# Performance work log

Hardware: AMD Instinct MI355X
Metric: run time of the kernel (lower is better)

The kernel has to match this reference:

```python
import jax, jax.numpy as jnp
import numpy as np
import math

B, C, BINS, W = 2, 8, 1024, 512
HEADS = 16
HD = BINS // HEADS          # 64 head dim
ROT = BINS // HEADS // 2    # 32 rotated dims
EXP = 4
EPS = 1e-5
MAX_FREQ = 10.0


def setup_inputs() -> dict:
    key = jax.random.key(0)
    ks = jax.random.split(key, 8)
    def u(k, shape, fan_in):
        lim = 1.0 / math.sqrt(fan_in)
        return jax.random.uniform(k, shape, jnp.float32, -lim, lim)
    return {
        "x": jax.random.normal(ks[0], (B, C, BINS, W), jnp.float32),
        "norm1_w": jnp.ones((BINS,), jnp.float32),
        "norm1_b": jnp.zeros((BINS,), jnp.float32),
        # 'pixel' rotary init: linspace(1, max_freq/2, dim//2) * pi (learned)
        "rot_freqs": jnp.linspace(1.0, MAX_FREQ / 2, ROT // 2, dtype=jnp.float32) * math.pi,
        "q_w": u(ks[1], (C, BINS, BINS), BINS),
        "out_w": u(ks[2], (C, BINS, BINS), BINS),
        "norm2_w": jnp.ones((BINS,), jnp.float32),
        "norm2_b": jnp.zeros((BINS,), jnp.float32),
        "lin1_w": u(ks[3], (C, BINS * EXP, BINS), BINS),
        "lin2_w": u(ks[4], (C, BINS, BINS * EXP), BINS * EXP),
    }


def _mlin(x, w):
    # x: [b,c,f_in,w]; w: [c,f_out,f_in] -> [b,c,f_out,w]
    return jnp.einsum('bcfw,cgf->bcgw', x, w)


def _frame_norm(x, w, b):
    # LayerNorm over the bins axis (axis=2) of [b,c,bins,w]
    m = jnp.mean(x, axis=2, keepdims=True)
    v = jnp.var(x, axis=2, keepdims=True)
    xn = (x - m) * jax.lax.rsqrt(v + EPS)
    return xn * w[:, None] + b[:, None]


def _rotate(q, cos, sin):
    # q: [b,c,h,w,d]; rotate first ROT dims with interleaved-pair rotate_half
    q1, q2 = q[..., :ROT], q[..., ROT:]
    qp = q1.reshape(*q1.shape[:-1], ROT // 2, 2)
    rh = jnp.stack([-qp[..., 1], qp[..., 0]], axis=-1).reshape(q1.shape)
    return jnp.concatenate([q1 * cos + rh * sin, q2], axis=-1)


def _attention(x, rot_freqs, q_w, out_w):
    b, c, bins, w = x.shape
    # faithful to source: q, k, v ALL use q_proj
    y = _mlin(x, q_w)  # [b,c,bins,w]
    # -> [b,c,h,w,d]
    y = y.transpose(0, 1, 3, 2).reshape(b, c, w, HEADS, HD).transpose(0, 1, 3, 2, 4)
    # rotary angles: t * freqs, repeat-interleaved x2 -> [w, ROT]
    t = jnp.arange(w, dtype=jnp.float32)
    ang = jnp.repeat(t[:, None] * rot_freqs[None, :], 2, axis=-1)
    cos, sin = jnp.cos(ang), jnp.sin(ang)
    q = _rotate(y, cos, sin)
    k = _rotate(y, cos, sin)
    v = y
    # NOTE: source scales by 1/sqrt(h) where h == bins (spectral height)
    scores = jnp.einsum('bchwd,bchud->bchwu', q, k) / math.sqrt(bins)
    a = jnp.einsum('bchwu,bchud->bchwd', jax.nn.softmax(scores, axis=-1), v)
    # [b,c,h,w,d] -> [b,c,bins,w]
    a = a.transpose(0, 1, 3, 2, 4).reshape(b, c, w, bins).transpose(0, 1, 3, 2)
    return _mlin(a, out_w)


def reference(x, norm1_w, norm1_b, rot_freqs, q_w, out_w,
              norm2_w, norm2_b, lin1_w, lin2_w):
    z = _frame_norm(x, norm1_w, norm1_b)
    z = _attention(z, rot_freqs, q_w, out_w)
    x = x + z  # dropout=0 -> identity
    z = _frame_norm(x, norm2_w, norm2_b)
    z = _mlin(jax.nn.gelu(_mlin(z, lin1_w), approximate=False), lin2_w)
    return x + z
```

## Files before the change

### kernel.cpp

```cpp
#include <hip/hip_runtime.h>
#include <math.h>

#define BB 2
#define CCH 8
#define BINS 1024
#define WW 512
#define HEADS 16
#define HD 64
#define ROTD 32
#define EXPF 4
#define NXE 8388608L
#define NTW 32

typedef unsigned short ushortT;
typedef short bf16x8 __attribute__((ext_vector_type(8)));
typedef float f32x4 __attribute__((ext_vector_type(4)));

__device__ __forceinline__ ushortT f2bf(float f) {
    unsigned int u = __float_as_uint(f);
    u = (u + 0x7FFF + ((u >> 16) & 1)) >> 16;
    return (ushortT)u;
}
__device__ __forceinline__ float bf2f(ushortT h) {
    return __uint_as_float(((unsigned int)h) << 16);
}
__device__ __forceinline__ float geluf(float x) {
    return 0.5f * x * (1.f + erff(x * 0.70710678118654752f));
}
__device__ __forceinline__ void gl_lds16(const ushortT* g, ushortT* l) {
    __builtin_amdgcn_global_load_lds(
        (const __attribute__((address_space(1))) unsigned int*)g,
        (__attribute__((address_space(3))) unsigned int*)l, 16, 0, 0);
}

__global__ __launch_bounds__(1024)
void normT_k(const float* __restrict__ X, const float* __restrict__ wgt,
             const float* __restrict__ bia, ushortT* __restrict__ YT)
{
    __shared__ float tile[NTW][BINS + 1];
    __shared__ float red0[32][NTW], red1[32][NTW];
    __shared__ float ms[NTW], is[NTW];
    const int bc = blockIdx.x >> 4;
    const int w0 = (blockIdx.x & 15) * NTW;
    const int tid = threadIdx.x;
    const int w  = tid & (NTW - 1);
    const int fy = tid >> 5;
    const float* Xb = X + (long)bc * BINS * WW + w0;
    float s = 0.f, s2 = 0.f;
    for (int f = fy; f < BINS; f += 32) {
        float v = Xb[(long)f * WW + w];
        s += v; s2 += v * v;
        tile[w][f] = v;
    }
    red0[fy][w] = s; red1[fy][w] = s2;
    __syncthreads();
    if (tid < NTW) {
        float ss = 0.f, qq = 0.f;
        #pragma unroll
        for (int j = 0; j < 32; ++j) { ss += red0[j][tid]; qq += red1[j][tid]; }
        float m = ss * (1.f / BINS);
        float var = qq * (1.f / BINS) - m * m;
        ms[tid] = m; is[tid] = rsqrtf(var + 1e-5f);
    }
    __syncthreads();
    const int w2 = tid >> 5;
    const int c  = tid & 31;
    float m = ms[w2], inv = is[w2];
    ushortT* Yb = YT + ((long)bc * WW + w0 + w2) * BINS;
    #pragma unroll
    for (int jj = 0; jj < 4; ++jj) {
        int f0 = jj * 256 + c * 8;
        union { ushortT h[8]; uint4 v; } r;
        #pragma unroll
        for (int e = 0; e < 8; ++e) {
            int f = f0 + e;
            float v = (tile[w2][f] - m) * inv * wgt[f] + bia[f];
            r.h[e] = f2bf(v);
        }
        *(uint4*)&Yb[f0] = r.v;
    }
}

__global__ void rope_tab_k(const float* __restrict__ freqs,
                           float* __restrict__ cosT, float* __restrict__ sinT)
{
    int idx = blockIdx.x * 256 + threadIdx.x;
    if (idx >= WW * 16) return;
    int w = idx >> 4, i = idx & 15;
    float ang = (float)w * freqs[i];
    cosT[idx] = cosf(ang);
    sinT[idx] = sinf(ang);
}

__global__ __launch_bounds__(256)
void ropeB_k(const ushortT* __restrict__ yT, const float* __restrict__ cosT,
             const float* __restrict__ sinT, ushortT* __restrict__ rotT)
{
    long e0 = ((long)blockIdx.x * 256 + threadIdx.x) * 8;
    if (e0 >= NXE) return;
    int g0 = (int)(e0 & 1023);
    int w  = (int)((e0 >> 10) & 511);
    int d0 = g0 & 63;
    union { uint4 v; ushortT h8[8]; } in, ov;
    in.v = *(const uint4*)&yT[e0];
    if (d0 >= ROTD) {
        *(uint4*)&rotT[e0] = in.v;
        return;
    }
    #pragma unroll
    for (int j = 0; j < 8; j += 2) {
        int i = (d0 + j) >> 1;
        float c = cosT[w * 16 + i], s = sinT[w * 16 + i];
        float a = bf2f(in.h8[j]), b = bf2f(in.h8[j + 1]);
        ov.h8[j]     = f2bf(a * c - b * s);
        ov.h8[j + 1] = f2bf(b * c + a * s);
    }
    *(uint4*)&rotT[e0] = ov.v;
}

__global__ __launch_bounds__(256)
void mattn_k(const ushortT* __restrict__ rotT, const ushortT* __restrict__ yT,
             ushortT* __restrict__ oT)
{
    __shared__ ushortT Qs[64 * 64];
    __shared__ ushortT Ks[64 * 64];
    __shared__ ushortT Vs[64 * 72];
    __shared__ ushortT Ps[64 * 72];
    const int z = blockIdx.y;
    const int bc = z >> 4, h = z & 15;
    const int wq0 = blockIdx.x * 64;
    const int tid = threadIdx.x;
    const int wv = tid >> 6, l = tid & 63;
    const int lr = l & 15, lk = l >> 4;
    const long hbase = (long)bc * WW * 1024 + h * 64;

    #pragma unroll
    for (int p = 0; p < 2; ++p) {
        int r0 = p * 32 + wv * 8;
        int row = r0 + (l >> 3);
        int gs = (l & 7) ^ (row & 7);
        gl_lds16(rotT + hbase + (long)(wq0 + row) * 1024 + gs * 8, Qs + r0 * 64);
    }

    f32x4 oacc[4] = {};
    float mrow[4] = {-INFINITY, -INFINITY, -INFINITY, -INFINITY};
    float lrow[4] = {0.f, 0.f, 0.f, 0.f};

    for (int u0 = 0; u0 < WW; u0 += 64) {
        #pragma unroll
        for (int p = 0; p < 2; ++p) {
            int r0 = p * 32 + wv * 8;
            int row = r0 + (l >> 3);
            int gs = (l & 7) ^ (row & 7);
            gl_lds16(rotT + hbase + (long)(u0 + row) * 1024 + gs * 8, Ks + r0 * 64);
        }
        #pragma unroll
        for (int rep = 0; rep < 2; ++rep) {
            int ch = rep * 4 + wv;
            union { uint4 v; ushortT h8[8]; } tmp;
            tmp.v = *(const uint4*)(yT + hbase + (long)(u0 + l) * 1024 + ch * 8);
            #pragma unroll
            for (int j = 0; j < 8; ++j)
                Vs[(ch * 8 + j) * 72 + l] = tmp.h8[j];
        }
        __syncthreads();

        f32x4 sacc[4] = {};
        #pragma unroll
        for (int ko = 0; ko < 2; ++ko) {
            int ar = wv * 16 + lr;
            bf16x8 aq = *(const bf16x8*)&Qs[ar * 64 + (((ko * 4) + lk) ^ (ar & 7)) * 8];
            #pragma unroll
            for (int f = 0; f < 4; ++f) {
                int br = f * 16 + lr;
                bf16x8 bk = *(const bf16x8*)&Ks[br * 64 + (((ko * 4) + lk) ^ (br & 7)) * 8];
                sacc[f] = __builtin_amdgcn_mfma_f32_16x16x32_bf16(aq, bk, sacc[f], 0, 0, 0);
            }
        }

        #pragma unroll
        for (int rg = 0; rg < 4; ++rg) {
            float s0 = sacc[0][rg] * (1.f / 32.f);
            float s1 = sacc[1][rg] * (1.f / 32.f);
            float s2 = sacc[2][rg] * (1.f / 32.f);
            float s3 = sacc[3][rg] * (1.f / 32.f);
            float mx = fmaxf(fmaxf(s0, s1), fmaxf(s2, s3));
            mx = fmaxf(mx, __shfl_xor(mx, 1));
            mx = fmaxf(mx, __shfl_xor(mx, 2));
            mx = fmaxf(mx, __shfl_xor(mx, 4));
            mx = fmaxf(mx, __shfl_xor(mx, 8));
            float mnew = fmaxf(mrow[rg], mx);
            float al = __expf(mrow[rg] - mnew);
            float p0 = __expf(s0 - mnew), p1 = __expf(s1 - mnew);
            float p2 = __expf(s2 - mnew), p3 = __expf(s3 - mnew);
            float rs = p0 + p1 + p2 + p3;
            rs += __shfl_xor(rs, 1);
            rs += __shfl_xor(rs, 2);
            rs += __shfl_xor(rs, 4);
            rs += __shfl_xor(rs, 8);
            lrow[rg] = lrow[rg] * al + rs;
            mrow[rg] = mnew;
            oacc[0][rg] *= al; oacc[1][rg] *= al;
            oacc[2][rg] *= al; oacc[3][rg] *= al;
            int prow = wv * 16 + lk * 4 + rg;
            Ps[prow * 72 +  0 + lr] = f2bf(p0);
            Ps[prow * 72 + 16 + lr] = f2bf(p1);
            Ps[prow * 72 + 32 + lr] = f2bf(p2);
            Ps[prow * 72 + 48 + lr] = f2bf(p3);
        }
        asm volatile("s_waitcnt lgkmcnt(0)" ::: "memory");

        #pragma unroll
        for (int ko = 0; ko < 2; ++ko) {
            int ar = wv * 16 + lr;
            bf16x8 ap = *(const bf16x8*)&Ps[ar * 72 + ko * 32 + lk * 8];
            #pragma unroll
            for (int f = 0; f < 4; ++f) {
                bf16x8 bv = *(const bf16x8*)&Vs[(f * 16 + lr) * 72 + ko * 32 + lk * 8];
                oacc[f] = __builtin_amdgcn_mfma_f32_16x16x32_bf16(ap, bv, oacc[f], 0, 0, 0);
            }
        }
        __syncthreads();
    }

    #pragma unroll
    for (int rg = 0; rg < 4; ++rg) {
        float inv = 1.f / lrow[rg];
        int w = wq0 + wv * 16 + lk * 4 + rg;
        long b2 = (long)bc * WW * 1024 + (long)w * 1024 + h * 64;
        #pragma unroll
        for (int f = 0; f < 4; ++f)
            oT[b2 + f * 16 + lr] = f2bf(oacc[f][rg] * inv);
    }
}

template<bool HASRES, bool GELUF, bool TRANSOUT>
__global__ __launch_bounds__(256)
void fgemm_k(const float* __restrict__ A, long sA, int aMod,
             const ushortT* __restrict__ B, long sB,
             void* __restrict__ Cp, long sC,
             const float* __restrict__ R, long sR,
             int M, int N, int K, int gx, int gy)
{
    __shared__ ushortT smem[4 * 8192];
    const int nwg = gridDim.x;
    const int bid = blockIdx.x;
    const int lid = (bid & 7) * (nwg >> 3) + (bid >> 3);
    const int x = lid % gx;
    const int y = (lid / gx) % gy;
    const int z = lid / (gx * gy);
    const float*   Ab = A + (long)(z % aMod) * sA + (long)y * 128 * K;
    const ushortT* Bb = B + (long)z * sB + (long)x * 128 * K;
    const int tid = threadIdx.x;
    const int wv = tid >> 6, l = tid & 63;
    const int lrow = l & 15, lk = l >> 4;
    const int mb = (wv >> 1) * 64, nb = (wv & 1) * 64;
    const int ar0 = tid >> 3 << 0;
    f32x4 acc[4][4] = {};
    float4 a0[4], a1[4];

    const int NT = K >> 6;

    auto fetchA = [&](int k0) {
        #pragma unroll
        for (int c = 0; c < 4; ++c) {
            int idx = tid + c * 256;
            int row = idx >> 3, grp = idx & 7;
            const float* src = Ab + (long)row * K + k0 + grp * 8;
            a0[c] = *(const float4*)src;
            a1[c] = *(const float4*)(src + 4);
        }
    };
    auto commitA = [&](int buf) {
        ushortT* AsB = smem + buf * 16384;
        #pragma unroll
        for (int c = 0; c < 4; ++c) {
            int idx = tid + c * 256;
            int row = idx >> 3, grp = idx & 7;
            union { ushortT h[8]; uint4 v; } r;
            r.h[0] = f2bf(a0[c].x); r.h[1] = f2bf(a0[c].y);
            r.h[2] = f2bf(a0[c].z); r.h[3] = f2bf(a0[c].w);
            r.h[4] = f2bf(a1[c].x); r.h[5] = f2bf(a1[c].y);
            r.h[6] = f2bf(a1[c].z); r.h[7] = f2bf(a1[c].w);
            *(uint4*)&AsB[row * 64 + ((grp ^ (row & 7)) << 3)] = r.v;
        }
    };
    auto stageB = [&](int buf, int k0) {
        ushortT* BsB = smem + 8192 + buf * 16384;
        #pragma unroll
        for (int t = 0; t < 4; ++t) {
            int r0 = wv * 32 + t * 8;
            int row = r0 + (l >> 3);
            int gs = (l & 7) ^ (row & 7);
            gl_lds16(Bb + (long)row * K + k0 + gs * 8, BsB + r0 * 64);
        }
    };
    auto compute = [&](int buf) {
        const ushortT* AsB = smem + buf * 16384;
        const ushortT* BsB = smem + 8192 + buf * 16384;
        #pragma unroll
        for (int ko = 0; ko < 2; ++ko) {
            bf16x8 af[4], bg[4];
            #pragma unroll
            for (int i = 0; i < 4; ++i) {
                int ra = mb + i * 16 + lrow;
                af[i] = *(const bf16x8*)&AsB[ra * 64 + ((lk + ko * 4) ^ (ra & 7)) * 8];
                int rb = nb + i * 16 + lrow;
                bg[i] = *(const bf16x8*)&BsB[rb * 64 + ((lk + ko * 4) ^ (rb & 7)) * 8];
            }
            #pragma unroll
            for (int i = 0; i < 4; ++i)
                #pragma unroll
                for (int j = 0; j < 4; ++j)
                    acc[i][j] = __builtin_amdgcn_mfma_f32_16x16x32_bf16(
                        af[i], bg[j], acc[i][j], 0, 0, 0);
        }
    };

    fetchA(0);
    stageB(0, 0);
    commitA(0);
    asm volatile("s_waitcnt vmcnt(0) lgkmcnt(0)" ::: "memory");
    __syncthreads();

    for (int t = 0; t < NT; ++t) {
        int buf = t & 1;
        if (t + 1 < NT) { fetchA((t + 1) << 6); stageB(buf ^ 1, (t + 1) << 6); }
        compute(buf);
        if (t + 1 < NT) {
            commitA(buf ^ 1);
            asm volatile("s_waitcnt vmcnt(0) lgkmcnt(0)" ::: "memory");
        }
        __syncthreads();
    }

    const int m0g = y * 128 + mb, n0g = x * 128 + nb;
    if (!TRANSOUT) {
        float* Cf = (float*)Cp + (long)z * sC;
        #pragma unroll
        for (int i = 0; i < 4; ++i)
            #pragma unroll
            for (int j = 0; j < 4; ++j)
                #pragma unroll
                for (int rg = 0; rg < 4; ++rg) {
                    long m = m0g + i * 16 + lk * 4 + rg;
                    long n = n0g + j * 16 + lrow;
                    float v = acc[i][j][rg];
                    if (GELUF) v = geluf(v);
                    if (HASRES) v += R[(long)z * sR + m * N + n];
                    Cf[m * N + n] = v;
                }
    } else {
        ushortT* Ts = smem + wv * 4096;
        __syncthreads();
        #pragma unroll
        for (int i = 0; i < 4; ++i)
            #pragma unroll
            for (int j = 0; j < 4; ++j)
                #pragma unroll
                for (int rg = 0; rg < 4; ++rg) {
                    int ml = i * 16 + lk * 4 + rg;
                    int nl = j * 16 + lrow;
                    float v = acc[i][j][rg];
                    if (GELUF) v = geluf(v);
                    Ts[nl * 64 + (((ml >> 3) ^ (nl & 7)) << 3) + (ml & 7)] = f2bf(v);
                }
        __syncthreads();
        ushortT* CT = (ushortT*)Cp + (long)z * sC;
        #pragma unroll
        for (int p = 0; p < 8; ++p) {
            int nl = p * 8 + (l >> 3), mc = l & 7;
            uint4 d = *(const uint4*)&Ts[nl * 64 + ((mc ^ (nl & 7)) << 3)];
            *(uint4*)&CT[(long)(n0g + nl) * M + m0g + mc * 8] = d;
        }
    }
}

extern "C" void kernel_launch(void* const* d_in, const int* in_sizes, int n_in,
                              void* d_out, int out_size, void* d_ws, size_t ws_size,
                              hipStream_t stream)
{
    const float* x    = (const float*)d_in[0];
    const float* n1w  = (const float*)d_in[1];
    const float* n1b  = (const float*)d_in[2];
    const float* freqs= (const float*)d_in[3];
    const float* qw   = (const float*)d_in[4];
    const float* ow   = (const float*)d_in[5];
    const float* n2w  = (const float*)d_in[6];
    const float* n2b  = (const float*)d_in[7];
    const float* l1w  = (const float*)d_in[8];
    const float* l2w  = (const float*)d_in[9];
    float* out = (float*)d_out;
    char* wsb  = (char*)d_ws;
    const long MB = 1L << 20;

    ushortT* znT  = (ushortT*)(wsb +   0 * MB);
    ushortT* yT   = (ushortT*)(wsb +  16 * MB);
    ushortT* rotT = (ushortT*)(wsb +  32 * MB);
    ushortT* CfT  = (ushortT*)(wsb +  48 * MB);
    ushortT* zn2T = (ushortT*)(wsb +  64 * MB);
    ushortT* h1T  = (ushortT*)(wsb +  80 * MB);
    float*   cosT = (float*)  (wsb + 144 * MB);
    float*   sinT = cosT + WW * 16;

    rope_tab_k<<<32, 256, 0, stream>>>(freqs, cosT, sinT);

    normT_k<<<BB * CCH * 16, 1024, 0, stream>>>(x, n1w, n1b, znT);

    fgemm_k<false, false, true><<<512, 256, 0, stream>>>(
        qw,  (long)BINS * BINS, CCH,
        znT, (long)WW * BINS,
        yT,  (long)WW * BINS,
        nullptr, 0, BINS, WW, BINS, 4, 8);

    ropeB_k<<<4096, 256, 0, stream>>>(yT, cosT, sinT, rotT);

    mattn_k<<<dim3(8, 256), 256, 0, stream>>>(rotT, yT, CfT);

    fgemm_k<true, false, false><<<512, 256, 0, stream>>>(
        ow,  (long)BINS * BINS, CCH,
        CfT, (long)WW * BINS,
        out, (long)BINS * WW,
        x,   (long)BINS * WW, BINS, WW, BINS, 4, 8);

    normT_k<<<BB * CCH * 16, 1024, 0, stream>>>(out, n2w, n2b, zn2T);

    fgemm_k<false, true, true><<<2048, 256, 0, stream>>>(
        l1w,  (long)BINS * EXPF * BINS, CCH,
        zn2T, (long)WW * BINS,
        h1T,  (long)WW * BINS * EXPF,
        nullptr, 0, BINS * EXPF, WW, BINS, 4, 32);

    fgemm_k<true, false, false><<<512, 256, 0, stream>>>(
        l2w, (long)BINS * BINS * EXPF, CCH,
        h1T, (long)WW * BINS * EXPF,
        out, (long)BINS * WW,
        out, (long)BINS * WW, BINS, WW, BINS * EXPF, 4, 8);
}
```

Baseline: 457.7 us.

## Single-buffer LDS in fgemm with explicit barriers and partial vmcnt waits

Cuts the GEMM's shared-memory footprint from a double buffer to a single buffer and restructures the main loop. Each iteration stages B and commits A, issues the next A global prefetch, waits only for the B loads via vmcnt(8), then computes. Halving LDS should allow more workgroups per CU for occupancy. The cost is losing the overlap of B loads with compute, plus an extra barrier per iteration, and the code now depends on hand-written waitcnt counts being correct.

```diff
diff --git a/kernel.cpp b/kernel.cpp
--- a/kernel.cpp
+++ b/kernel.cpp
@@ -242,7 +242,9 @@
              const float* __restrict__ R, long sR,
              int M, int N, int K, int gx, int gy)
 {
-    __shared__ ushortT smem[4 * 8192];
+    __shared__ ushortT smem[2 * 8192];
+    ushortT* As = smem;
+    ushortT* Bs = smem + 8192;
     const int nwg = gridDim.x;
     const int bid = blockIdx.x;
     const int lid = (bid & 7) * (nwg >> 3) + (bid >> 3);
@@ -255,58 +257,50 @@
     const int wv = tid >> 6, l = tid & 63;
     const int lrow = l & 15, lk = l >> 4;
     const int mb = (wv >> 1) * 64, nb = (wv & 1) * 64;
-    const int ar0 = tid >> 3 << 0;
+    const int arow = tid >> 3, agrp = tid & 7;
     f32x4 acc[4][4] = {};
     float4 a0[4], a1[4];
-
     const int NT = K >> 6;
 
     auto fetchA = [&](int k0) {
         #pragma unroll
         for (int c = 0; c < 4; ++c) {
-            int idx = tid + c * 256;
-            int row = idx >> 3, grp = idx & 7;
-            const float* src = Ab + (long)row * K + k0 + grp * 8;
+            const float* src = Ab + (long)(arow + c * 32) * K + k0 + agrp * 8;
             a0[c] = *(const float4*)src;
             a1[c] = *(const float4*)(src + 4);
         }
     };
-    auto commitA = [&](int buf) {
-        ushortT* AsB = smem + buf * 16384;
+    auto commitA = [&]() {
         #pragma unroll
         for (int c = 0; c < 4; ++c) {
-            int idx = tid + c * 256;
-            int row = idx >> 3, grp = idx & 7;
+            int row = arow + c * 32;
             union { ushortT h[8]; uint4 v; } r;
             r.h[0] = f2bf(a0[c].x); r.h[1] = f2bf(a0[c].y);
             r.h[2] = f2bf(a0[c].z); r.h[3] = f2bf(a0[c].w);
             r.h[4] = f2bf(a1[c].x); r.h[5] = f2bf(a1[c].y);
             r.h[6] = f2bf(a1[c].z); r.h[7] = f2bf(a1[c].w);
-            *(uint4*)&AsB[row * 64 + ((grp ^ (row & 7)) << 3)] = r.v;
+            *(uint4*)&As[row * 64 + ((agrp ^ (row & 7)) << 3)] = r.v;
         }
     };
-    auto stageB = [&](int buf, int k0) {
-        ushortT* BsB = smem + 8192 + buf * 16384;
+    auto stageB = [&](int k0) {
         #pragma unroll
         for (int t = 0; t < 4; ++t) {
             int r0 = wv * 32 + t * 8;
             int row = r0 + (l >> 3);
             int gs = (l & 7) ^ (row & 7);
-            gl_lds16(Bb + (long)row * K + k0 + gs * 8, BsB + r0 * 64);
+            gl_lds16(Bb + (long)row * K + k0 + gs * 8, Bs + r0 * 64);
         }
     };
-    auto compute = [&](int buf) {
-        const ushortT* AsB = smem + buf * 16384;
-        const ushortT* BsB = smem + 8192 + buf * 16384;
+    auto compute = [&]() {
         #pragma unroll
         for (int ko = 0; ko < 2; ++ko) {
             bf16x8 af[4], bg[4];
             #pragma unroll
             for (int i = 0; i < 4; ++i) {
                 int ra = mb + i * 16 + lrow;
-                af[i] = *(const bf16x8*)&AsB[ra * 64 + ((lk + ko * 4) ^ (ra & 7)) * 8];
+                af[i] = *(const bf16x8*)&As[ra * 64 + ((lk + ko * 4) ^ (ra & 7)) * 8];
                 int rb = nb + i * 16 + lrow;
-                bg[i] = *(const bf16x8*)&BsB[rb * 64 + ((lk + ko * 4) ^ (rb & 7)) * 8];
+                bg[i] = *(const bf16x8*)&Bs[rb * 64 + ((lk + ko * 4) ^ (rb & 7)) * 8];
             }
             #pragma unroll
             for (int i = 0; i < 4; ++i)
@@ -318,20 +312,23 @@
     };
 
     fetchA(0);
-    stageB(0, 0);
-    commitA(0);
-    asm volatile("s_waitcnt vmcnt(0) lgkmcnt(0)" ::: "memory");
-    __syncthreads();
-
     for (int t = 0; t < NT; ++t) {
-        int buf = t & 1;
-        if (t + 1 < NT) { fetchA((t + 1) << 6); stageB(buf ^ 1, (t + 1) << 6); }
-        compute(buf);
+        __builtin_amdgcn_s_barrier();
+        __builtin_amdgcn_sched_barrier(0);
+        stageB(t << 6);
+        __builtin_amdgcn_sched_barrier(0);
+        commitA();
         if (t + 1 < NT) {
-            commitA(buf ^ 1);
+            fetchA((t + 1) << 6);
+            __builtin_amdgcn_sched_barrier(0);
+            asm volatile("s_waitcnt vmcnt(8) lgkmcnt(0)" ::: "memory");
+        } else {
+            __builtin_amdgcn_sched_barrier(0);
             asm volatile("s_waitcnt vmcnt(0) lgkmcnt(0)" ::: "memory");
         }
-        __syncthreads();
+        __builtin_amdgcn_s_barrier();
+        __builtin_amdgcn_sched_barrier(0);
+        compute();
     }
 
     const int m0g = y * 128 + mb, n0g = x * 128 + nb;
```

Result: faster. 436.4 us (-4.7%).
